# Performance work log

Hardware: AMD Instinct MI355X
Metric: run time of the kernel (lower is better)

Reference implementation:

```python
import jax, jax.numpy as jnp
import numpy as np

N = 4096          # number_of_node
DIN = 3           # dim_input (forced: fc1 expects N*dim_input == N*3 after last stage)
DOUT = 4          # dim_output
DACT = N          # dim_action defaults to number_of_node
B = 128


def setup_inputs() -> dict:
    key = jax.random.key(0)
    ks = jax.random.split(key, 12)
    X = jax.random.normal(ks[0], (B, N * DIN), dtype=jnp.float32)
    adj = jax.random.uniform(ks[1], (N, N), dtype=jnp.float32)
    def lin(kw, kb, fan_in, fan_out):
        bound = 1.0 / np.sqrt(fan_in)
        W = jax.random.uniform(kw, (fan_in, fan_out), minval=-bound, maxval=bound, dtype=jnp.float32)
        b = jax.random.uniform(kb, (fan_out,), minval=-bound, maxval=bound, dtype=jnp.float32)
        return W, b
    W1, b1 = lin(ks[2], ks[3], DIN, 4)
    W2, b2 = lin(ks[4], ks[5], 4, DOUT)
    W3, b3 = lin(ks[6], ks[7], DOUT, 3)
    Wfc, bfc = lin(ks[8], ks[9], N * DIN, 54)
    Wout, bout = lin(ks[10], ks[11], 54, DACT)
    return {"X": X, "adj": adj, "W1": W1, "b1": b1, "W2": W2, "b2": b2,
            "W3": W3, "b3": b3, "Wfc": Wfc, "bfc": bfc, "Wout": Wout, "bout": bout}


def reference(X, adj, W1, b1, W2, b2, W3, b3, Wfc, bfc, Wout, bout):
    # X: [B, N*DIN] -> [B, N, DIN]
    h = X.reshape(X.shape[0], N, DIN)
    # three (adj @ h) aggregations fused with tiny Linear + ReLU
    h = jax.nn.relu(jnp.einsum('nm,bmf->bnf', adj, h) @ W1 + b1)   # [B,N,4]
    h = jax.nn.relu(jnp.einsum('nm,bmf->bnf', adj, h) @ W2 + b2)   # [B,N,DOUT]
    h = jax.nn.relu(jnp.einsum('nm,bmf->bnf', adj, h) @ W3 + b3)   # [B,N,3]
    flat = h.reshape(h.shape[0], -1)                               # [B, N*3]
    hid = jax.nn.relu(flat @ Wfc + bfc)                            # [B, 54]
    q_value = hid @ Wout + bout                                    # [B, DACT]
    return q_value
```

## Files before the change

kernel.cpp:

```cpp
#include <hip/hip_runtime.h>


typedef __bf16 bf16x8 __attribute__((ext_vector_type(8)));
typedef float  f32x4  __attribute__((ext_vector_type(4)));

#define N_NODE 4096
#define BATCH  128

__device__ __forceinline__ void async_copy16(const void* gsrc, void* ldst) {
    __builtin_amdgcn_global_load_lds(
        (const __attribute__((address_space(1))) void*)gsrc,
        (__attribute__((address_space(3))) void*)ldst,
        16, 0, 0);
}

__global__ __launch_bounds__(256) void prep_k(const float* __restrict__ adj,
                                              __bf16* __restrict__ adjB,
                                              const float* __restrict__ X,
                                              const float* __restrict__ W1,
                                              __bf16* __restrict__ G0,
                                              float* __restrict__ hid_acc) {
    const int blk = blockIdx.x, tx = threadIdx.x;
    if (blk < 8192) {
        const size_t i = (size_t)blk * 256 + tx;
        const float4* a4 = (const float4*)adj;
        float4 u = a4[i * 2];
        float4 v = a4[i * 2 + 1];
        bf16x8 o = { (__bf16)u.x, (__bf16)u.y, (__bf16)u.z, (__bf16)u.w,
                     (__bf16)v.x, (__bf16)v.y, (__bf16)v.z, (__bf16)v.w };
        *(bf16x8*)(adjB + i * 8) = o;
    } else if (blk < 10240) {
        const int base = (blk - 8192) * 1024;
        const int c = base >> 12, b = c >> 2, f = c & 3;
        const float w0 = W1[0 * 4 + f], w1 = W1[1 * 4 + f], w2 = W1[2 * 4 + f];
        const float* Xb = X + (size_t)b * 12288;
#pragma unroll
        for (int k = 0; k < 4; ++k) {
            const int idx = base + k * 256 + tx;
            const int m = idx & 4095;
            const float v = Xb[m * 3 + 0] * w0 + Xb[m * 3 + 1] * w1 + Xb[m * 3 + 2] * w2;
            G0[idx] = (__bf16)v;
        }
    } else {
        const int i = (blk - 10240) * 256 + tx;
        if (i < BATCH * 54) hid_acc[i] = 0.f;
    }
}

template <int MODE>
__global__ __launch_bounds__(256) void gcn_k(const __bf16* __restrict__ A,
                                             const __bf16* __restrict__ Bt,
                                             const float* __restrict__ Wa,
                                             const float* __restrict__ ba,
                                             const float* __restrict__ Wb,
                                             __bf16* __restrict__ Hout,
                                             float* __restrict__ H3out) {
    __shared__ __align__(16) unsigned char smem[65536];
    const int tx   = threadIdx.x;
    const int wave = tx >> 6, lane = tx & 63;
    const int quad = lane >> 4, lr = lane & 15;

    const int l = blockIdx.x;
    const int xcd = l & 7, s = l >> 3;
    const int mi = xcd * 8 + (s & 7), ci = s >> 3;
    const int m0 = mi * 64, c0 = ci * 64;

    const __bf16* gA[4];
    const __bf16* gB[4];
#pragma unroll
    for (int q = 0; q < 4; ++q) {
        const int c = q * 256 + tx;
        const int r = c >> 4, p = c & 15;
        const int lk = (p - (r & 15)) & 15;
        gA[q] = A  + (size_t)(m0 + r) * 4096 + lk * 8;
        gB[q] = Bt + (size_t)(c0 + r) * 4096 + lk * 8;
    }

    const int posw = ((wave * 4 + quad + lr) & 15) * 8;
    int foff[4];
#pragma unroll
    for (int g = 0; g < 4; ++g) foff[g] = (g * 16 + lr) * 128 + posw;

    f32x4 acc[4][4] = {};

#pragma unroll
    for (int q = 0; q < 4; ++q) {
        async_copy16(gA[q], smem + q * 4096 + tx * 16);
        async_copy16(gB[q], smem + 16384 + q * 4096 + tx * 16);
    }

    int buf = 0;
    for (int kt = 0; kt < 32; ++kt) {
        __syncthreads();
        if (kt + 1 < 32) {
            const int k0 = (kt + 1) * 128;
            const int bo = (buf ^ 1) * 32768;
#pragma unroll
            for (int q = 0; q < 4; ++q) {
                async_copy16(gA[q] + k0, smem + bo + q * 4096 + tx * 16);
                async_copy16(gB[q] + k0, smem + bo + 16384 + q * 4096 + tx * 16);
            }
        }
        const __bf16* Ab = (const __bf16*)(smem + buf * 32768);
        const __bf16* Bb = (const __bf16*)(smem + buf * 32768 + 16384);
        bf16x8 af[4], bv[4];
#pragma unroll
        for (int i = 0; i < 4; ++i) af[i] = *(const bf16x8*)(Ab + foff[i]);
#pragma unroll
        for (int j = 0; j < 4; ++j) bv[j] = *(const bf16x8*)(Bb + foff[j]);
#pragma unroll
        for (int i = 0; i < 4; ++i)
#pragma unroll
            for (int j = 0; j < 4; ++j)
                acc[i][j] = __builtin_amdgcn_mfma_f32_16x16x32_bf16(af[i], bv[j], acc[i][j], 0, 0, 0);
        buf ^= 1;
    }

    __syncthreads();
    float* part = (float*)smem;
    if (wave != 0) {
        float* slot = part + (wave - 1) * 4096;
#pragma unroll
        for (int t = 0; t < 16; ++t)
            *(f32x4*)(slot + lane * 64 + ((t + lane) & 15) * 4) = acc[t >> 2][t & 3];
    }
    __syncthreads();
    float* Ct = (float*)(smem + 32768);
    if (wave == 0) {
#pragma unroll
        for (int t = 0; t < 16; ++t) {
            const int o = lane * 64 + ((t + lane) & 15) * 4;
            f32x4 p0 = *(const f32x4*)(part + o);
            f32x4 p1 = *(const f32x4*)(part + 4096 + o);
            f32x4 p2 = *(const f32x4*)(part + 8192 + o);
            acc[t >> 2][t & 3] += p0 + p1 + p2;
        }
#pragma unroll
        for (int i = 0; i < 4; ++i)
#pragma unroll
            for (int j = 0; j < 4; ++j)
#pragma unroll
                for (int r = 0; r < 4; ++r)
                    Ct[(i * 16 + quad * 4 + r) * 65 + j * 16 + lr] = acc[i][j][r];
    }
    __syncthreads();

    const int m_l = tx & 63, bq = tx >> 6;
    if (MODE == 0) {
        const float b0f = ba[0], b1f = ba[1], b2f = ba[2], b3f = ba[3];
#pragma unroll
        for (int q = 0; q < 4; ++q) {
            const int bl = bq * 4 + q;
            const float* row = &Ct[m_l * 65 + bl * 4];
            __bf16* o = Hout + (size_t)(c0 + bl * 4) * N_NODE + m0 + m_l;
            o[0 * N_NODE] = (__bf16)fmaxf(row[0] + b0f, 0.f);
            o[1 * N_NODE] = (__bf16)fmaxf(row[1] + b1f, 0.f);
            o[2 * N_NODE] = (__bf16)fmaxf(row[2] + b2f, 0.f);
            o[3 * N_NODE] = (__bf16)fmaxf(row[3] + b3f, 0.f);
        }
    } else if (MODE == 1) {
        float W2l[16], W3l[12], bl2[4];
#pragma unroll
        for (int i = 0; i < 16; ++i) W2l[i] = Wa[i];
#pragma unroll
        for (int i = 0; i < 12; ++i) W3l[i] = Wb[i];
#pragma unroll
        for (int i = 0; i < 4; ++i) bl2[i] = ba[i];
#pragma unroll
        for (int q = 0; q < 4; ++q) {
            const int bl = bq * 4 + q;
            const float* row = &Ct[m_l * 65 + bl * 4];
            float tmp[4];
#pragma unroll
            for (int fo = 0; fo < 4; ++fo)
                tmp[fo] = fmaxf(row[0] * W2l[fo] + row[1] * W2l[4 + fo] +
                                row[2] * W2l[8 + fo] + row[3] * W2l[12 + fo] + bl2[fo], 0.f);
            __bf16* o = Hout + (size_t)(c0 + bl * 4) * N_NODE + m0 + m_l;
#pragma unroll
            for (int f3 = 0; f3 < 3; ++f3)
                o[f3 * N_NODE] = (__bf16)(tmp[0] * W3l[f3] + tmp[1] * W3l[3 + f3] +
                                          tmp[2] * W3l[6 + f3] + tmp[3] * W3l[9 + f3]);
            o[3 * N_NODE] = (__bf16)0.f;
        }
    } else {
        const float b0f = ba[0], b1f = ba[1], b2f = ba[2];
#pragma unroll
        for (int q = 0; q < 4; ++q) {
            const int bl = bq * 4 + q;
            const int b = ci * 16 + bl;
            const float* row = &Ct[m_l * 65 + bl * 4];
            float* o = H3out + (size_t)(b * 3) * N_NODE + m0 + m_l;
            o[0 * N_NODE] = fmaxf(row[0] + b0f, 0.f);
            o[1 * N_NODE] = fmaxf(row[1] + b1f, 0.f);
            o[2 * N_NODE] = fmaxf(row[2] + b2f, 0.f);
        }
    }
}

__global__ __launch_bounds__(256) void fc1p_k(const float* __restrict__ H3,
                                              const float* __restrict__ Wfc,
                                              float* __restrict__ hid_acc) {
    __shared__ float hs[16 * 192];
    __shared__ float red[4][16][64];
    const int tx = threadIdx.x;
    const int wv = tx >> 6, lane = tx & 63;
    const int n0 = blockIdx.x * 64;
    const int b0 = blockIdx.y * 16;

    for (int idx = tx; idx < 3072; idx += 256) {
        const int n = idx & 63, f = (idx >> 6) % 3, b = idx / 192;
        hs[idx] = H3[((size_t)((b0 + b) * 3 + f)) * N_NODE + n0 + n];
    }
    __syncthreads();

    float acc[16];
#pragma unroll
    for (int b = 0; b < 16; ++b) acc[b] = 0.f;
    if (lane < 54) {
        const int nb = wv * 16;
        for (int n = 0; n < 16; ++n) {
#pragma unroll
            for (int f = 0; f < 3; ++f) {
                const float w = Wfc[((size_t)(n0 + nb + n) * 3 + f) * 54 + lane];
#pragma unroll
                for (int b = 0; b < 16; ++b)
                    acc[b] += hs[b * 192 + f * 64 + nb + n] * w;
            }
        }
    }
#pragma unroll
    for (int b = 0; b < 16; ++b) red[wv][b][lane] = acc[b];
    __syncthreads();
    if (wv == 0 && lane < 54) {
        for (int b = 0; b < 16; ++b) {
            const float s = red[0][b][lane] + red[1][b][lane] +
                            red[2][b][lane] + red[3][b][lane];
            atomicAdd(&hid_acc[(b0 + b) * 54 + lane], s);
        }
    }
}

__global__ __launch_bounds__(256) void fc2_k(const float* __restrict__ hid_acc,
                                             const float* __restrict__ bfc,
                                             const float* __restrict__ Wout,
                                             const float* __restrict__ bout,
                                             float* __restrict__ out) {
    const int tx = threadIdx.x;
    const int a  = blockIdx.x * 256 + tx;
    const int b0 = blockIdx.y * 4;
    __shared__ float hs[4 * 54];
    if (tx < 216) {
        const int j = tx % 54;
        hs[tx] = fmaxf(hid_acc[b0 * 54 + tx] + bfc[j], 0.f);
    }
    __syncthreads();
    float a0 = 0.f, a1 = 0.f, a2 = 0.f, a3 = 0.f;
    for (int j = 0; j < 54; ++j) {
        float w = Wout[(size_t)j * N_NODE + a];
        a0 += hs[0 * 54 + j] * w;
        a1 += hs[1 * 54 + j] * w;
        a2 += hs[2 * 54 + j] * w;
        a3 += hs[3 * 54 + j] * w;
    }
    float bo = bout[a];
    out[(size_t)(b0 + 0) * N_NODE + a] = a0 + bo;
    out[(size_t)(b0 + 1) * N_NODE + a] = a1 + bo;
    out[(size_t)(b0 + 2) * N_NODE + a] = a2 + bo;
    out[(size_t)(b0 + 3) * N_NODE + a] = a3 + bo;
}

extern "C" void kernel_launch(void* const* d_in, const int* in_sizes, int n_in,
                              void* d_out, int out_size, void* d_ws, size_t ws_size,
                              hipStream_t stream) {
    const float* X    = (const float*)d_in[0];
    const float* adj  = (const float*)d_in[1];
    const float* W1   = (const float*)d_in[2];
    const float* b1   = (const float*)d_in[3];
    const float* W2   = (const float*)d_in[4];
    const float* b2   = (const float*)d_in[5];
    const float* W3   = (const float*)d_in[6];
    const float* b3   = (const float*)d_in[7];
    const float* Wfc  = (const float*)d_in[8];
    const float* bfc  = (const float*)d_in[9];
    const float* Wout = (const float*)d_in[10];
    const float* bout = (const float*)d_in[11];
    float* out = (float*)d_out;

    char* w = (char*)d_ws;
    __bf16* adjB = (__bf16*)w;
    __bf16* G0   = (__bf16*)(w + 33554432);
    __bf16* H1   = (__bf16*)(w + 33554432 + 4194304);
    __bf16* H2g  = (__bf16*)(w + 33554432 + 2 * 4194304);
    float*  H3   = (float*)(w + 33554432 + 3 * 4194304);
    float*  hid  = (float*)(w + 33554432 + 3 * 4194304 + 6291456);

    prep_k<<<10267, 256, 0, stream>>>(adj, adjB, X, W1, G0, hid);

    gcn_k<0><<<512, 256, 0, stream>>>(adjB, G0, nullptr, b1, nullptr, H1, nullptr);
    gcn_k<1><<<512, 256, 0, stream>>>(adjB, H1, W2, b2, W3, H2g, nullptr);
    gcn_k<2><<<512, 256, 0, stream>>>(adjB, H2g, nullptr, b3, nullptr, nullptr, H3);

    fc1p_k<<<dim3(64, 8), 256, 0, stream>>>(H3, Wfc, hid);
    fc2_k<<<dim3(16, 32), 256, 0, stream>>>(hid, bfc, Wout, bout, out);
}
```

Measured before the change: 223.9 us.

## Prepack B operand in MFMA fragment layout and enlarge GCN tile to 128 rows

The intermediate activations G0/H1/H2 are now written in a pre-swizzled fragment layout, so each wave loads its B fragments straight from global memory into registers instead of staging them through LDS. The GEMM block becomes 512 threads covering 128 adjacency rows, with waves split along M and K, a tree reduction of the K-split partials, and s_setprio around the MFMA bursts. The intent is to halve LDS staging traffic, reuse each B fragment across more rows of A, and overlap loads with MFMA work. In exchange it uses more registers, adds extra barriers for the reduction, and makes the epilogue indexing more complex.

```diff
diff --git a/kernel.cpp b/kernel.cpp
--- a/kernel.cpp
+++ b/kernel.cpp
@@ -29,134 +29,157 @@
         bf16x8 o = { (__bf16)u.x, (__bf16)u.y, (__bf16)u.z, (__bf16)u.w,
                      (__bf16)v.x, (__bf16)v.y, (__bf16)v.z, (__bf16)v.w };
         *(bf16x8*)(adjB + i * 8) = o;
-    } else if (blk < 10240) {
-        const int base = (blk - 8192) * 1024;
-        const int c = base >> 12, b = c >> 2, f = c & 3;
+    } else if (blk < 9216) {
+        const int g = (blk - 8192) * 256 + tx;
+        const int lp = g & 63, cbg = (g >> 6) & 31, kc = g >> 11;
+        const int c = cbg * 16 + (lp & 15);
+        const int b = c >> 2, f = c & 3;
         const float w0 = W1[0 * 4 + f], w1 = W1[1 * 4 + f], w2 = W1[2 * 4 + f];
-        const float* Xb = X + (size_t)b * 12288;
-#pragma unroll
-        for (int k = 0; k < 4; ++k) {
-            const int idx = base + k * 256 + tx;
-            const int m = idx & 4095;
-            const float v = Xb[m * 3 + 0] * w0 + Xb[m * 3 + 1] * w1 + Xb[m * 3 + 2] * w2;
-            G0[idx] = (__bf16)v;
-        }
+        const int mb = kc * 32 + ((lp >> 4) & 3) * 8;
+        const float* Xb = X + (size_t)b * 12288 + (size_t)mb * 3;
+        bf16x8 o;
+#pragma unroll
+        for (int j = 0; j < 8; ++j) {
+            const float v = Xb[j * 3 + 0] * w0 + Xb[j * 3 + 1] * w1 + Xb[j * 3 + 2] * w2;
+            o[j] = (__bf16)v;
+        }
+        *(bf16x8*)(G0 + (size_t)g * 8) = o;
     } else {
-        const int i = (blk - 10240) * 256 + tx;
+        const int i = (blk - 9216) * 256 + tx;
         if (i < BATCH * 54) hid_acc[i] = 0.f;
     }
 }
 
 template <int MODE>
-__global__ __launch_bounds__(256) void gcn_k(const __bf16* __restrict__ A,
-                                             const __bf16* __restrict__ Bt,
-                                             const float* __restrict__ Wa,
-                                             const float* __restrict__ ba,
-                                             const float* __restrict__ Wb,
-                                             __bf16* __restrict__ Hout,
-                                             float* __restrict__ H3out) {
+__global__ __launch_bounds__(512, 2) void gcn_k(const __bf16* __restrict__ A,
+                                                const __bf16* __restrict__ Bp,
+                                                const float* __restrict__ Wa,
+                                                const float* __restrict__ ba,
+                                                const float* __restrict__ Wb,
+                                                __bf16* __restrict__ Op,
+                                                float* __restrict__ H3out) {
     __shared__ __align__(16) unsigned char smem[65536];
-    const int tx   = threadIdx.x;
+    const int tx = threadIdx.x;
     const int wave = tx >> 6, lane = tx & 63;
     const int quad = lane >> 4, lr = lane & 15;
+    const int wm = wave >> 2, wk = wave & 3;
 
     const int l = blockIdx.x;
     const int xcd = l & 7, s = l >> 3;
-    const int mi = xcd * 8 + (s & 7), ci = s >> 3;
-    const int m0 = mi * 64, c0 = ci * 64;
+    const int mi = xcd * 4 + (s & 3), ci = s >> 2;
+    const int m0 = mi * 128, c0 = ci * 64;
 
     const __bf16* gA[4];
+#pragma unroll
+    for (int q = 0; q < 4; ++q) {
+        const int c = q * 512 + tx;
+        const int r = c >> 4, p = c & 15;
+        const int lk = (p - r) & 15;
+        gA[q] = A + (size_t)(m0 + r) * 4096 + lk * 8;
+    }
     const __bf16* gB[4];
 #pragma unroll
-    for (int q = 0; q < 4; ++q) {
-        const int c = q * 256 + tx;
-        const int r = c >> 4, p = c & 15;
-        const int lk = (p - (r & 15)) & 15;
-        gA[q] = A  + (size_t)(m0 + r) * 4096 + lk * 8;
-        gB[q] = Bt + (size_t)(c0 + r) * 4096 + lk * 8;
-    }
-
-    const int posw = ((wave * 4 + quad + lr) & 15) * 8;
-    int foff[4];
-#pragma unroll
-    for (int g = 0; g < 4; ++g) foff[g] = (g * 16 + lr) * 128 + posw;
+    for (int j = 0; j < 4; ++j)
+        gB[j] = Bp + ((size_t)((wk * 32 + (ci * 4 + j)) * 64 + lane)) * 8;
+
+    const int posw = ((wk * 4 + quad + lr) & 15) * 8;
+    int foffA[4];
+#pragma unroll
+    for (int i = 0; i < 4; ++i) foffA[i] = (wm * 64 + i * 16 + lr) * 128 + posw;
 
     f32x4 acc[4][4] = {};
-
-#pragma unroll
-    for (int q = 0; q < 4; ++q) {
-        async_copy16(gA[q], smem + q * 4096 + tx * 16);
-        async_copy16(gB[q], smem + 16384 + q * 4096 + tx * 16);
-    }
-
-    int buf = 0;
-    for (int kt = 0; kt < 32; ++kt) {
-        __syncthreads();
-        if (kt + 1 < 32) {
-            const int k0 = (kt + 1) * 128;
-            const int bo = (buf ^ 1) * 32768;
-#pragma unroll
-            for (int q = 0; q < 4; ++q) {
-                async_copy16(gA[q] + k0, smem + bo + q * 4096 + tx * 16);
-                async_copy16(gB[q] + k0, smem + bo + 16384 + q * 4096 + tx * 16);
-            }
-        }
-        const __bf16* Ab = (const __bf16*)(smem + buf * 32768);
-        const __bf16* Bb = (const __bf16*)(smem + buf * 32768 + 16384);
-        bf16x8 af[4], bv[4];
-#pragma unroll
-        for (int i = 0; i < 4; ++i) af[i] = *(const bf16x8*)(Ab + foff[i]);
-#pragma unroll
-        for (int j = 0; j < 4; ++j) bv[j] = *(const bf16x8*)(Bb + foff[j]);
-#pragma unroll
-        for (int i = 0; i < 4; ++i)
-#pragma unroll
-            for (int j = 0; j < 4; ++j)
-                acc[i][j] = __builtin_amdgcn_mfma_f32_16x16x32_bf16(af[i], bv[j], acc[i][j], 0, 0, 0);
-        buf ^= 1;
-    }
+    bf16x8 bv0[4], bv1[4];
+
+#pragma unroll
+    for (int q = 0; q < 4; ++q)
+        async_copy16(gA[q], smem + q * 8192 + tx * 16);
+#pragma unroll
+    for (int j = 0; j < 4; ++j) bv0[j] = *(const bf16x8*)(gB[j]);
+
+#define GCN_ITER(KT, CUR, NXT)                                                 \
+    {                                                                          \
+        asm volatile("s_waitcnt vmcnt(0)" ::: "memory");                       \
+        __builtin_amdgcn_s_barrier();                                          \
+        const __bf16* Ab = (const __bf16*)(smem + ((KT) & 1) * 32768);         \
+        bf16x8 af[4];                                                          \
+        _Pragma("unroll") for (int i = 0; i < 4; ++i)                          \
+            af[i] = *(const bf16x8*)(Ab + foffA[i]);                           \
+        if ((KT) + 1 < 32) {                                                   \
+            const int bo = (((KT) + 1) & 1) * 32768;                           \
+            const int k0 = ((KT) + 1) * 128;                                   \
+            _Pragma("unroll") for (int q = 0; q < 4; ++q)                      \
+                async_copy16(gA[q] + k0, smem + bo + q * 8192 + tx * 16);      \
+            _Pragma("unroll") for (int j = 0; j < 4; ++j)                      \
+                NXT[j] = *(const bf16x8*)(gB[j] + ((KT) + 1) * 65536);         \
+        }                                                                      \
+        __builtin_amdgcn_s_setprio(1);                                         \
+        _Pragma("unroll") for (int i = 0; i < 4; ++i)                          \
+            _Pragma("unroll") for (int j = 0; j < 4; ++j)                      \
+                acc[i][j] = __builtin_amdgcn_mfma_f32_16x16x32_bf16(           \
+                    af[i], CUR[j], acc[i][j], 0, 0, 0);                        \
+        __builtin_amdgcn_s_setprio(0);                                         \
+    }
+
+    for (int kt = 0; kt < 32; kt += 2) {
+        GCN_ITER(kt, bv0, bv1)
+        GCN_ITER(kt + 1, bv1, bv0)
+    }
+#undef GCN_ITER
 
     __syncthreads();
     float* part = (float*)smem;
-    if (wave != 0) {
-        float* slot = part + (wave - 1) * 4096;
+    if (wk & 1) {
+        float* slot = part + (wm * 2 + (wk >> 1)) * 4096;
 #pragma unroll
         for (int t = 0; t < 16; ++t)
             *(f32x4*)(slot + lane * 64 + ((t + lane) & 15) * 4) = acc[t >> 2][t & 3];
     }
     __syncthreads();
-    float* Ct = (float*)(smem + 32768);
-    if (wave == 0) {
-#pragma unroll
-        for (int t = 0; t < 16; ++t) {
-            const int o = lane * 64 + ((t + lane) & 15) * 4;
-            f32x4 p0 = *(const f32x4*)(part + o);
-            f32x4 p1 = *(const f32x4*)(part + 4096 + o);
-            f32x4 p2 = *(const f32x4*)(part + 8192 + o);
-            acc[t >> 2][t & 3] += p0 + p1 + p2;
-        }
+    if (!(wk & 1)) {
+        const float* slot = part + (wm * 2 + (wk >> 1)) * 4096;
+#pragma unroll
+        for (int t = 0; t < 16; ++t)
+            acc[t >> 2][t & 3] += *(const f32x4*)(slot + lane * 64 + ((t + lane) & 15) * 4);
+    }
+    __syncthreads();
+    if (wk == 2) {
+        float* slot = part + wm * 4096;
+#pragma unroll
+        for (int t = 0; t < 16; ++t)
+            *(f32x4*)(slot + lane * 64 + ((t + lane) & 15) * 4) = acc[t >> 2][t & 3];
+    }
+    __syncthreads();
+    if (wk == 0) {
+#pragma unroll
+        for (int t = 0; t < 16; ++t)
+            acc[t >> 2][t & 3] += *(const f32x4*)(part + wm * 4096 + lane * 64 + ((t + lane) & 15) * 4);
+    }
+    __syncthreads();
+    float* Ct = part;
+    if (wk == 0) {
 #pragma unroll
         for (int i = 0; i < 4; ++i)
 #pragma unroll
             for (int j = 0; j < 4; ++j)
 #pragma unroll
                 for (int r = 0; r < 4; ++r)
-                    Ct[(i * 16 + quad * 4 + r) * 65 + j * 16 + lr] = acc[i][j][r];
-    }
-    __syncthreads();
-
-    const int m_l = tx & 63, bq = tx >> 6;
+                    Ct[(wm * 64 + i * 16 + quad * 4 + r) * 65 + j * 16 + lr] = acc[i][j][r];
+    }
+    __syncthreads();
+
     if (MODE == 0) {
-        const float b0f = ba[0], b1f = ba[1], b2f = ba[2], b3f = ba[3];
-#pragma unroll
-        for (int q = 0; q < 4; ++q) {
-            const int bl = bq * 4 + q;
-            const float* row = &Ct[m_l * 65 + bl * 4];
-            __bf16* o = Hout + (size_t)(c0 + bl * 4) * N_NODE + m0 + m_l;
-            o[0 * N_NODE] = (__bf16)fmaxf(row[0] + b0f, 0.f);
-            o[1 * N_NODE] = (__bf16)fmaxf(row[1] + b1f, 0.f);
-            o[2 * N_NODE] = (__bf16)fmaxf(row[2] + b2f, 0.f);
-            o[3 * N_NODE] = (__bf16)fmaxf(row[3] + b3f, 0.f);
+#pragma unroll
+        for (int it = 0; it < 2; ++it) {
+            const int g = it * 512 + tx;
+            const int lp = g & 63, cbl = (g >> 6) & 3, kcl = g >> 8;
+            const int cl = cbl * 16 + (lp & 15);
+            const float bf = ba[cl & 3];
+            const int mb = kcl * 32 + ((lp >> 4) & 3) * 8;
+            bf16x8 o;
+#pragma unroll
+            for (int j = 0; j < 8; ++j)
+                o[j] = (__bf16)fmaxf(Ct[(mb + j) * 65 + cl] + bf, 0.f);
+            *(bf16x8*)(Op + ((size_t)((mi * 4 + kcl) * 32 + (ci * 4 + cbl)) * 64 + lp) * 8) = o;
         }
     } else if (MODE == 1) {
         float W2l[16], W3l[12], bl2[4];
@@ -167,32 +190,41 @@
 #pragma unroll
         for (int i = 0; i < 4; ++i) bl2[i] = ba[i];
 #pragma unroll
-        for (int q = 0; q < 4; ++q) {
-            const int bl = bq * 4 + q;
-            const float* row = &Ct[m_l * 65 + bl * 4];
-            float tmp[4];
-#pragma unroll
-            for (int fo = 0; fo < 4; ++fo)
-                tmp[fo] = fmaxf(row[0] * W2l[fo] + row[1] * W2l[4 + fo] +
-                                row[2] * W2l[8 + fo] + row[3] * W2l[12 + fo] + bl2[fo], 0.f);
-            __bf16* o = Hout + (size_t)(c0 + bl * 4) * N_NODE + m0 + m_l;
-#pragma unroll
-            for (int f3 = 0; f3 < 3; ++f3)
-                o[f3 * N_NODE] = (__bf16)(tmp[0] * W3l[f3] + tmp[1] * W3l[3 + f3] +
-                                          tmp[2] * W3l[6 + f3] + tmp[3] * W3l[9 + f3]);
-            o[3 * N_NODE] = (__bf16)0.f;
+        for (int it = 0; it < 2; ++it) {
+            const int g = it * 512 + tx;
+            const int lp = g & 63, cbl = (g >> 6) & 3, kcl = g >> 8;
+            const int cl = cbl * 16 + (lp & 15);
+            const int bloc = cl >> 2, f3 = cl & 3;
+            const int mb = kcl * 32 + ((lp >> 4) & 3) * 8;
+            bf16x8 o;
+#pragma unroll
+            for (int j = 0; j < 8; ++j) {
+                const float* row = &Ct[(mb + j) * 65 + bloc * 4];
+                float v = 0.f;
+                if (f3 < 3) {
+#pragma unroll
+                    for (int fo = 0; fo < 4; ++fo) {
+                        const float tmp = fmaxf(row[0] * W2l[fo] + row[1] * W2l[4 + fo] +
+                                                row[2] * W2l[8 + fo] + row[3] * W2l[12 + fo] +
+                                                bl2[fo], 0.f);
+                        const float w3a = W3l[fo * 3 + 0], w3b = W3l[fo * 3 + 1],
+                                    w3c = W3l[fo * 3 + 2];
+                        v += tmp * (f3 == 0 ? w3a : (f3 == 1 ? w3b : w3c));
+                    }
+                }
+                o[j] = (__bf16)v;
+            }
+            *(bf16x8*)(Op + ((size_t)((mi * 4 + kcl) * 32 + (ci * 4 + cbl)) * 64 + lp) * 8) = o;
         }
     } else {
-        const float b0f = ba[0], b1f = ba[1], b2f = ba[2];
-#pragma unroll
-        for (int q = 0; q < 4; ++q) {
-            const int bl = bq * 4 + q;
-            const int b = ci * 16 + bl;
-            const float* row = &Ct[m_l * 65 + bl * 4];
-            float* o = H3out + (size_t)(b * 3) * N_NODE + m0 + m_l;
-            o[0 * N_NODE] = fmaxf(row[0] + b0f, 0.f);
-            o[1 * N_NODE] = fmaxf(row[1] + b1f, 0.f);
-            o[2 * N_NODE] = fmaxf(row[2] + b2f, 0.f);
+        const int m_l = tx & 127, cq = tx >> 7;
+#pragma unroll
+        for (int t = 0; t < 16; ++t) {
+            const int cl = cq * 16 + t;
+            const int c = c0 + cl, b = c >> 2, f = c & 3;
+            if (f < 3)
+                H3out[(size_t)(b * 3 + f) * N_NODE + m0 + m_l] =
+                    fmaxf(Ct[m_l * 65 + cl] + ba[f], 0.f);
         }
     }
 }
@@ -294,11 +326,11 @@
     float*  H3   = (float*)(w + 33554432 + 3 * 4194304);
     float*  hid  = (float*)(w + 33554432 + 3 * 4194304 + 6291456);
 
-    prep_k<<<10267, 256, 0, stream>>>(adj, adjB, X, W1, G0, hid);
-
-    gcn_k<0><<<512, 256, 0, stream>>>(adjB, G0, nullptr, b1, nullptr, H1, nullptr);
-    gcn_k<1><<<512, 256, 0, stream>>>(adjB, H1, W2, b2, W3, H2g, nullptr);
-    gcn_k<2><<<512, 256, 0, stream>>>(adjB, H2g, nullptr, b3, nullptr, nullptr, H3);
+    prep_k<<<9243, 256, 0, stream>>>(adj, adjB, X, W1, G0, hid);
+
+    gcn_k<0><<<256, 512, 0, stream>>>(adjB, G0, nullptr, b1, nullptr, H1, nullptr);
+    gcn_k<1><<<256, 512, 0, stream>>>(adjB, H1, W2, b2, W3, H2g, nullptr);
+    gcn_k<2><<<256, 512, 0, stream>>>(adjB, H2g, nullptr, b3, nullptr, nullptr, H3);
 
     fc1p_k<<<dim3(64, 8), 256, 0, stream>>>(H3, Wfc, hid);
     fc2_k<<<dim3(16, 32), 256, 0, stream>>>(hid, bfc, Wout, bout, out);
```

After: 248.3 us. 10.9% more time.
